# Kernel optimization log

Hardware: AMD Instinct MI355X
Metric: run time of the kernel (lower is better)

## Reference

```python
import jax, jax.numpy as jnp
import numpy as np

B, N_HOP, N_MEM, DIM = 1024, 2, 32, 64


def setup_inputs() -> dict:
    key = jax.random.key(0)
    ks = jax.random.split(key, 8)
    # Xavier-ish scales for linear weights
    def xav(k, shape):
        fan_in = shape[-1]
        return jax.random.normal(k, shape, dtype=jnp.float32) * (1.0 / np.sqrt(fan_in))
    return {
        "hs": jax.random.normal(ks[0], (B, N_HOP, N_MEM, DIM), dtype=jnp.float32),
        "Rs": jax.random.normal(ks[1], (B, N_HOP, N_MEM, DIM, DIM), dtype=jnp.float32) * (1.0 / np.sqrt(DIM)),
        "ts": jax.random.normal(ks[2], (B, N_HOP, N_MEM, DIM), dtype=jnp.float32),
        "vs": jax.random.normal(ks[3], (B, DIM), dtype=jnp.float32),
        "W1_w": xav(ks[4], (DIM, 4 * DIM)),
        "W1_b": jnp.zeros((DIM,), dtype=jnp.float32),
        "W2_w": xav(ks[5], (1, DIM)),
        "W2_b": jnp.zeros((1,), dtype=jnp.float32),
        "Wmem_w": xav(ks[6], (N_HOP, DIM, 3 * DIM)),
        "Wmem_b": jnp.zeros((N_HOP, DIM), dtype=jnp.float32),
        "z_w": xav(ks[7], (DIM, 2 * DIM)),
        "z_b": jnp.zeros((DIM,), dtype=jnp.float32),
    }


def reference(hs, Rs, ts, vs, W1_w, W1_b, W2_w, W2_b, Wmem_w, Wmem_b, z_w, z_b):
    """Faithful RippleNetPlus.forward (eval mode: dropout is identity)."""
    M = vs  # prev_mem
    o = vs  # v passed into EpisodicMemory each hop
    n_hop = hs.shape[1]
    for hop in range(n_hop):
        R = Rs[:, hop]   # [B, M, D, D]
        h = hs[:, hop]   # [B, M, D]
        t = ts[:, hop]   # [B, M, D]
        # batched GEMV replacing the B*n_memory Python-loop matmuls
        Rh = jnp.einsum('bmde,bme->bmd', R, h)  # [B, M, D]
        v = o[:, None, :]       # [B, 1, D]
        pm = M[:, None, :]      # [B, 1, D]
        z = jnp.concatenate(
            [Rh * v, Rh * pm, jnp.abs(Rh - v), jnp.abs(Rh - pm)], axis=-1)  # [B, M, 4D]
        hcode = jnp.tanh(jnp.einsum('bmf,df->bmd', z, W1_w) + W1_b)
        Z = (jnp.einsum('bmd,od->bmo', hcode, W2_w) + W2_b)[..., 0]  # [B, M]
        g = jax.nn.softmax(Z, axis=1)[..., None]                     # [B, M, 1]
        o_new = jnp.sum(t * g, axis=1)                               # [B, D]
        concat = jnp.concatenate([M, o_new, o], axis=1)              # [B, 3D]
        M = jax.nn.relu(concat @ Wmem_w[hop].T + Wmem_b[hop])
        o = o_new
    # AnswerModule
    u = jnp.concatenate([M, vs], axis=1) @ z_w.T + z_b  # [B, D]
    return jnp.sum(vs * u, axis=1)  # [B]
```

## Files before the change

### kernel.cpp

```cpp
#include <hip/hip_runtime.h>
#include <math.h>

#define NHOP 2
#define MEM 32
#define DIM 64

typedef __attribute__((ext_vector_type(8))) short short8v;
typedef __attribute__((ext_vector_type(4))) float f32x4;

__device__ __forceinline__ float fast_tanh(float x) {
    const float e = __expf(2.f * x);
    return 1.f - 2.f / (e + 1.f);
}

__device__ __forceinline__ short bf16b(float x) {
    union { float f; unsigned u; } c; c.f = x;
    const unsigned r = c.u + 0x7fffu + ((c.u >> 16) & 1u);
    return (short)(r >> 16);
}

__global__ __launch_bounds__(256, 3) void ripple_fwd(
    const float* __restrict__ hs,
    const float* __restrict__ Rs,
    const float* __restrict__ ts,
    const float* __restrict__ vs,
    const float* __restrict__ W1_w,
    const float* __restrict__ W1_b,
    const float* __restrict__ W2_w,
    const float* __restrict__ W2_b,
    const float* __restrict__ Wmem_w,
    const float* __restrict__ Wmem_b,
    const float* __restrict__ z_w,
    const float* __restrict__ z_b,
    float* __restrict__ out)
{
    __shared__ uint4 W1B[32 * 64];
    __shared__ float Rh_sm[MEM][68];
    __shared__ float part[4][32][17];
    __shared__ float M_sm[DIM], o_sm[DIM], onew_sm[DIM], vs_sm[DIM];
    __shared__ float Zp[2][MEM];
    __shared__ float cvec[128];

    const int b   = blockIdx.x;
    const int tid = threadIdx.x;
    const int l   = tid & 63;
    const int wv  = tid >> 6;

    #pragma unroll
    for (int t = 0; t < 8; ++t) {
        const int s    = t * 256 + tid;
        const int frag = s >> 6, ll = s & 63;
        const int kt = frag >> 2, nt = frag & 3;
        const int n  = nt * 16 + (ll & 15);
        const int f0 = kt * 32 + (ll >> 4) * 8;
        const float4 wa = *reinterpret_cast<const float4*>(W1_w + n * 256 + f0);
        const float4 wb = *reinterpret_cast<const float4*>(W1_w + n * 256 + f0 + 4);
        short8v v;
        v[0] = bf16b(wa.x); v[1] = bf16b(wa.y); v[2] = bf16b(wa.z); v[3] = bf16b(wa.w);
        v[4] = bf16b(wb.x); v[5] = bf16b(wb.y); v[6] = bf16b(wb.z); v[7] = bf16b(wb.w);
        *reinterpret_cast<short8v*>(&W1B[s]) = v;
    }
    if (tid < DIM) {
        cvec[tid]      = W1_b[tid];
        cvec[64 + tid] = W2_w[tid];
        const float v = vs[b * DIM + tid];
        M_sm[tid] = v; o_sm[tid] = v; vs_sm[tid] = v;
    }

    const int s4   = l & 15;
    const int dq   = l >> 4;
    const int rrow = l & 31;
    const int hi   = l >> 5;

    for (int hop = 0; hop < NHOP; ++hop) {
        const float* __restrict__ Rbase = Rs + (size_t)(b * NHOP + hop) * MEM * DIM * DIM;
        const float* __restrict__ hbase = hs + (size_t)(b * NHOP + hop) * MEM * DIM;
        const float* __restrict__ tbase = ts + (size_t)(b * NHOP + hop) * MEM * DIM;

        #pragma unroll 2
        for (int k = 0; k < 8; ++k) {
            const int m = k * 4 + wv;
            const float* __restrict__ Rm = Rbase + (size_t)m * DIM * DIM;
            const float4 hv = *reinterpret_cast<const float4*>(hbase + m * DIM + 4 * s4);
            #pragma unroll
            for (int half = 0; half < 2; ++half) {
                #pragma unroll
                for (int i = 0; i < 8; ++i) {
                    const float4 r = *reinterpret_cast<const float4*>(
                        Rm + (half * 8 + i) * 256 + 4 * l);
                    const float p = r.x*hv.x + r.y*hv.y + r.z*hv.z + r.w*hv.w;
                    part[wv][4 * i + dq][s4] = p;
                }
                float a = 0.f;
                #pragma unroll
                for (int j = 0; j < 8; ++j)
                    a += part[wv][rrow][hi * 8 + j];
                a += __shfl_xor(a, 32);
                if (l < 32) Rh_sm[m][half * 32 + rrow] = a;
            }
        }
        __syncthreads();

        {
            const int g   = l >> 4;
            const int col = l & 15;
            const int mt  = wv & 1;
            const int nh  = wv >> 1;
            const int m   = mt * 16 + col;
            f32x4 acc0 = {0.f, 0.f, 0.f, 0.f};
            f32x4 acc1 = {0.f, 0.f, 0.f, 0.f};
            #pragma unroll
            for (int kt = 0; kt < 8; ++kt) {
                const int part2 = kt >> 1;
                const int e0 = (kt & 1) * 32 + g * 8;
                const float4 r0 = *reinterpret_cast<const float4*>(&Rh_sm[m][e0]);
                const float4 r1 = *reinterpret_cast<const float4*>(&Rh_sm[m][e0 + 4]);
                const float* vsrc = (part2 & 1) ? M_sm : o_sm;
                const float4 q0 = *reinterpret_cast<const float4*>(vsrc + e0);
                const float4 q1 = *reinterpret_cast<const float4*>(vsrc + e0 + 4);
                float zz[8];
                if (part2 < 2) {
                    zz[0] = r0.x*q0.x; zz[1] = r0.y*q0.y; zz[2] = r0.z*q0.z; zz[3] = r0.w*q0.w;
                    zz[4] = r1.x*q1.x; zz[5] = r1.y*q1.y; zz[6] = r1.z*q1.z; zz[7] = r1.w*q1.w;
                } else {
                    zz[0] = fabsf(r0.x-q0.x); zz[1] = fabsf(r0.y-q0.y);
                    zz[2] = fabsf(r0.z-q0.z); zz[3] = fabsf(r0.w-q0.w);
                    zz[4] = fabsf(r1.x-q1.x); zz[5] = fabsf(r1.y-q1.y);
                    zz[6] = fabsf(r1.z-q1.z); zz[7] = fabsf(r1.w-q1.w);
                }
                short8v a;
                a[0] = bf16b(zz[0]); a[1] = bf16b(zz[1]); a[2] = bf16b(zz[2]); a[3] = bf16b(zz[3]);
                a[4] = bf16b(zz[4]); a[5] = bf16b(zz[5]); a[6] = bf16b(zz[6]); a[7] = bf16b(zz[7]);
                const short8v b0 = *reinterpret_cast<const short8v*>(&W1B[(kt * 4 + nh * 2 + 0) * 64 + l]);
                const short8v b1 = *reinterpret_cast<const short8v*>(&W1B[(kt * 4 + nh * 2 + 1) * 64 + l]);
                acc0 = __builtin_amdgcn_mfma_f32_16x16x32_bf16(a, b0, acc0, 0, 0, 0);
                acc1 = __builtin_amdgcn_mfma_f32_16x16x32_bf16(a, b1, acc1, 0, 0, 0);
            }
            const int n0 = (nh * 2 + 0) * 16 + col;
            const int n1 = (nh * 2 + 1) * 16 + col;
            const float b1a = cvec[n0], b1b = cvec[n1];
            const float w2a = cvec[64 + n0], w2b = cvec[64 + n1];
            float pz[4];
            #pragma unroll
            for (int r = 0; r < 4; ++r)
                pz[r] = fast_tanh(acc0[r] + b1a) * w2a + fast_tanh(acc1[r] + b1b) * w2b;
            #pragma unroll
            for (int s = 1; s < 16; s <<= 1) {
                pz[0] += __shfl_xor(pz[0], s, 64);
                pz[1] += __shfl_xor(pz[1], s, 64);
                pz[2] += __shfl_xor(pz[2], s, 64);
                pz[3] += __shfl_xor(pz[3], s, 64);
            }
            if (col == 0) {
                #pragma unroll
                for (int r = 0; r < 4; ++r)
                    Zp[nh][mt * 16 + 4 * g + r] = pz[r];
            }
        }
        __syncthreads();

        if (tid < DIM) {
            float mx = -1e30f;
            #pragma unroll
            for (int m = 0; m < MEM; ++m) mx = fmaxf(mx, Zp[0][m] + Zp[1][m]);
            float s = 0.f, accn = 0.f;
            #pragma unroll
            for (int m = 0; m < MEM; ++m) {
                const float e = __expf(Zp[0][m] + Zp[1][m] - mx);
                s += e;
                accn = fmaf(tbase[m * DIM + tid], e, accn);
            }
            const float onew = accn / s;
            onew_sm[tid] = onew;

            const float* __restrict__ Wm = Wmem_w + (size_t)(hop * DIM + tid) * 192;
            float acc2 = Wmem_b[hop * DIM + tid];
            #pragma unroll
            for (int k = 0; k < 16; ++k) {
                const float4 w = *reinterpret_cast<const float4*>(Wm + 4 * k);
                acc2 += w.x * M_sm[4*k] + w.y * M_sm[4*k+1] + w.z * M_sm[4*k+2] + w.w * M_sm[4*k+3];
            }
            #pragma unroll
            for (int k = 0; k < 16; ++k) {
                const float4 w = *reinterpret_cast<const float4*>(Wm + 64 + 4 * k);
                acc2 += w.x * onew_sm[4*k] + w.y * onew_sm[4*k+1] + w.z * onew_sm[4*k+2] + w.w * onew_sm[4*k+3];
            }
            #pragma unroll
            for (int k = 0; k < 16; ++k) {
                const float4 w = *reinterpret_cast<const float4*>(Wm + 128 + 4 * k);
                acc2 += w.x * o_sm[4*k] + w.y * o_sm[4*k+1] + w.z * o_sm[4*k+2] + w.w * o_sm[4*k+3];
            }
            M_sm[tid] = fmaxf(acc2, 0.f);
            o_sm[tid] = onew;
        }
        if (hop == 0) __syncthreads();
    }

    if (tid < DIM) {
        const float* __restrict__ zr = z_w + (size_t)tid * 128;
        float u = z_b[tid];
        #pragma unroll
        for (int k = 0; k < 16; ++k) {
            const float4 w = *reinterpret_cast<const float4*>(zr + 4 * k);
            u += w.x * M_sm[4*k] + w.y * M_sm[4*k+1] + w.z * M_sm[4*k+2] + w.w * M_sm[4*k+3];
        }
        #pragma unroll
        for (int k = 0; k < 16; ++k) {
            const float4 w = *reinterpret_cast<const float4*>(zr + 64 + 4 * k);
            u += w.x * vs_sm[4*k] + w.y * vs_sm[4*k+1] + w.z * vs_sm[4*k+2] + w.w * vs_sm[4*k+3];
        }
        float r = vs_sm[tid] * u;
        #pragma unroll
        for (int s = 1; s < 64; s <<= 1) r += __shfl_xor(r, s, 64);
        if (tid == 0) out[b] = r;
    }
}

extern "C" void kernel_launch(void* const* d_in, const int* in_sizes, int n_in,
                              void* d_out, int out_size, void* d_ws, size_t ws_size,
                              hipStream_t stream)
{
    const float* hs     = (const float*)d_in[0];
    const float* Rs     = (const float*)d_in[1];
    const float* ts     = (const float*)d_in[2];
    const float* vs     = (const float*)d_in[3];
    const float* W1_w   = (const float*)d_in[4];
    const float* W1_b   = (const float*)d_in[5];
    const float* W2_w   = (const float*)d_in[6];
    const float* W2_b   = (const float*)d_in[7];
    const float* Wmem_w = (const float*)d_in[8];
    const float* Wmem_b = (const float*)d_in[9];
    const float* z_w    = (const float*)d_in[10];
    const float* z_b    = (const float*)d_in[11];
    float* out = (float*)d_out;

    const int B = out_size;
    ripple_fwd<<<B, 256, 0, stream>>>(hs, Rs, ts, vs, W1_w, W1_b, W2_w, W2_b,
                                      Wmem_w, Wmem_b, z_w, z_b, out);
}
```

Before: 195.3 us.

## Overlap hop-0 memory update with hop-1 Rh GEMV via warp specialization

```diff
diff --git a/kernel.cpp b/kernel.cpp
--- a/kernel.cpp
+++ b/kernel.cpp
@@ -36,7 +36,7 @@
 {
     __shared__ uint4 W1B[32 * 64];
     __shared__ float Rh_sm[MEM][68];
-    __shared__ float part[4][32][17];
+    __shared__ __align__(16) float part[4][32][20];
     __shared__ float M_sm[DIM], o_sm[DIM], onew_sm[DIM], vs_sm[DIM];
     __shared__ float Zp[2][MEM];
     __shared__ float cvec[128];
@@ -72,93 +72,92 @@
     const int rrow = l & 31;
     const int hi   = l >> 5;
 
-    for (int hop = 0; hop < NHOP; ++hop) {
-        const float* __restrict__ Rbase = Rs + (size_t)(b * NHOP + hop) * MEM * DIM * DIM;
-        const float* __restrict__ hbase = hs + (size_t)(b * NHOP + hop) * MEM * DIM;
-        const float* __restrict__ tbase = ts + (size_t)(b * NHOP + hop) * MEM * DIM;
-
-        #pragma unroll 2
-        for (int k = 0; k < 8; ++k) {
-            const int m = k * 4 + wv;
-            const float* __restrict__ Rm = Rbase + (size_t)m * DIM * DIM;
-            const float4 hv = *reinterpret_cast<const float4*>(hbase + m * DIM + 4 * s4);
-            #pragma unroll
-            for (int half = 0; half < 2; ++half) {
-                #pragma unroll
-                for (int i = 0; i < 8; ++i) {
-                    const float4 r = *reinterpret_cast<const float4*>(
-                        Rm + (half * 8 + i) * 256 + 4 * l);
-                    const float p = r.x*hv.x + r.y*hv.y + r.z*hv.z + r.w*hv.w;
-                    part[wv][4 * i + dq][s4] = p;
-                }
-                float a = 0.f;
-                #pragma unroll
-                for (int j = 0; j < 8; ++j)
-                    a += part[wv][rrow][hi * 8 + j];
-                a += __shfl_xor(a, 32);
-                if (l < 32) Rh_sm[m][half * 32 + rrow] = a;
-            }
-        }
-        __syncthreads();
-
-        {
-            const int g   = l >> 4;
-            const int col = l & 15;
-            const int mt  = wv & 1;
-            const int nh  = wv >> 1;
-            const int m   = mt * 16 + col;
-            f32x4 acc0 = {0.f, 0.f, 0.f, 0.f};
-            f32x4 acc1 = {0.f, 0.f, 0.f, 0.f};
-            #pragma unroll
-            for (int kt = 0; kt < 8; ++kt) {
-                const int part2 = kt >> 1;
-                const int e0 = (kt & 1) * 32 + g * 8;
-                const float4 r0 = *reinterpret_cast<const float4*>(&Rh_sm[m][e0]);
-                const float4 r1 = *reinterpret_cast<const float4*>(&Rh_sm[m][e0 + 4]);
-                const float* vsrc = (part2 & 1) ? M_sm : o_sm;
-                const float4 q0 = *reinterpret_cast<const float4*>(vsrc + e0);
-                const float4 q1 = *reinterpret_cast<const float4*>(vsrc + e0 + 4);
-                float zz[8];
-                if (part2 < 2) {
-                    zz[0] = r0.x*q0.x; zz[1] = r0.y*q0.y; zz[2] = r0.z*q0.z; zz[3] = r0.w*q0.w;
-                    zz[4] = r1.x*q1.x; zz[5] = r1.y*q1.y; zz[6] = r1.z*q1.z; zz[7] = r1.w*q1.w;
-                } else {
-                    zz[0] = fabsf(r0.x-q0.x); zz[1] = fabsf(r0.y-q0.y);
-                    zz[2] = fabsf(r0.z-q0.z); zz[3] = fabsf(r0.w-q0.w);
-                    zz[4] = fabsf(r1.x-q1.x); zz[5] = fabsf(r1.y-q1.y);
-                    zz[6] = fabsf(r1.z-q1.z); zz[7] = fabsf(r1.w-q1.w);
-                }
-                short8v a;
-                a[0] = bf16b(zz[0]); a[1] = bf16b(zz[1]); a[2] = bf16b(zz[2]); a[3] = bf16b(zz[3]);
-                a[4] = bf16b(zz[4]); a[5] = bf16b(zz[5]); a[6] = bf16b(zz[6]); a[7] = bf16b(zz[7]);
-                const short8v b0 = *reinterpret_cast<const short8v*>(&W1B[(kt * 4 + nh * 2 + 0) * 64 + l]);
-                const short8v b1 = *reinterpret_cast<const short8v*>(&W1B[(kt * 4 + nh * 2 + 1) * 64 + l]);
-                acc0 = __builtin_amdgcn_mfma_f32_16x16x32_bf16(a, b0, acc0, 0, 0, 0);
-                acc1 = __builtin_amdgcn_mfma_f32_16x16x32_bf16(a, b1, acc1, 0, 0, 0);
-            }
-            const int n0 = (nh * 2 + 0) * 16 + col;
-            const int n1 = (nh * 2 + 1) * 16 + col;
-            const float b1a = cvec[n0], b1b = cvec[n1];
-            const float w2a = cvec[64 + n0], w2b = cvec[64 + n1];
-            float pz[4];
+    const float* __restrict__ Rbase0 = Rs + (size_t)(b * NHOP + 0) * MEM * DIM * DIM;
+    const float* __restrict__ Rbase1 = Rs + (size_t)(b * NHOP + 1) * MEM * DIM * DIM;
+    const float* __restrict__ hbase0 = hs + (size_t)(b * NHOP + 0) * MEM * DIM;
+    const float* __restrict__ hbase1 = hs + (size_t)(b * NHOP + 1) * MEM * DIM;
+    const float* __restrict__ tbase0 = ts + (size_t)(b * NHOP + 0) * MEM * DIM;
+    const float* __restrict__ tbase1 = ts + (size_t)(b * NHOP + 1) * MEM * DIM;
+
+    auto p1 = [&](const float* __restrict__ Rbase, const float* __restrict__ hbase,
+                  const int m) {
+        const float* __restrict__ Rm = Rbase + (size_t)m * DIM * DIM;
+        const float4 hv = *reinterpret_cast<const float4*>(hbase + m * DIM + 4 * s4);
+        #pragma unroll
+        for (int half = 0; half < 2; ++half) {
+            #pragma unroll
+            for (int i = 0; i < 8; ++i) {
+                const f32x4* rp = reinterpret_cast<const f32x4*>(
+                    Rm + (half * 8 + i) * 256 + 4 * l);
+                const f32x4 r = __builtin_nontemporal_load(rp);
+                part[wv][4 * i + dq][s4] = r.x*hv.x + r.y*hv.y + r.z*hv.z + r.w*hv.w;
+            }
+            const float4 pa = *reinterpret_cast<const float4*>(&part[wv][rrow][hi * 8]);
+            const float4 pb = *reinterpret_cast<const float4*>(&part[wv][rrow][hi * 8 + 4]);
+            float a = ((pa.x + pa.y) + (pa.z + pa.w)) + ((pb.x + pb.y) + (pb.z + pb.w));
+            a += __shfl_xor(a, 32);
+            if (l < 32) Rh_sm[m][half * 32 + rrow] = a;
+        }
+    };
+
+    auto p2 = [&]() {
+        const int g   = l >> 4;
+        const int col = l & 15;
+        const int mt  = wv & 1;
+        const int nh  = wv >> 1;
+        const int m   = mt * 16 + col;
+        f32x4 acc0 = {0.f, 0.f, 0.f, 0.f};
+        f32x4 acc1 = {0.f, 0.f, 0.f, 0.f};
+        #pragma unroll
+        for (int kt = 0; kt < 8; ++kt) {
+            const int pt = kt >> 1;
+            const int e0 = (kt & 1) * 32 + g * 8;
+            const float4 r0 = *reinterpret_cast<const float4*>(&Rh_sm[m][e0]);
+            const float4 r1 = *reinterpret_cast<const float4*>(&Rh_sm[m][e0 + 4]);
+            const float* vsrc = (pt & 1) ? M_sm : o_sm;
+            const float4 q0 = *reinterpret_cast<const float4*>(vsrc + e0);
+            const float4 q1 = *reinterpret_cast<const float4*>(vsrc + e0 + 4);
+            float zz[8];
+            if (pt < 2) {
+                zz[0] = r0.x*q0.x; zz[1] = r0.y*q0.y; zz[2] = r0.z*q0.z; zz[3] = r0.w*q0.w;
+                zz[4] = r1.x*q1.x; zz[5] = r1.y*q1.y; zz[6] = r1.z*q1.z; zz[7] = r1.w*q1.w;
+            } else {
+                zz[0] = fabsf(r0.x-q0.x); zz[1] = fabsf(r0.y-q0.y);
+                zz[2] = fabsf(r0.z-q0.z); zz[3] = fabsf(r0.w-q0.w);
+                zz[4] = fabsf(r1.x-q1.x); zz[5] = fabsf(r1.y-q1.y);
+                zz[6] = fabsf(r1.z-q1.z); zz[7] = fabsf(r1.w-q1.w);
+            }
+            short8v a;
+            a[0] = bf16b(zz[0]); a[1] = bf16b(zz[1]); a[2] = bf16b(zz[2]); a[3] = bf16b(zz[3]);
+            a[4] = bf16b(zz[4]); a[5] = bf16b(zz[5]); a[6] = bf16b(zz[6]); a[7] = bf16b(zz[7]);
+            const short8v b0 = *reinterpret_cast<const short8v*>(&W1B[(kt * 4 + nh * 2 + 0) * 64 + l]);
+            const short8v b1 = *reinterpret_cast<const short8v*>(&W1B[(kt * 4 + nh * 2 + 1) * 64 + l]);
+            acc0 = __builtin_amdgcn_mfma_f32_16x16x32_bf16(a, b0, acc0, 0, 0, 0);
+            acc1 = __builtin_amdgcn_mfma_f32_16x16x32_bf16(a, b1, acc1, 0, 0, 0);
+        }
+        const int n0 = (nh * 2 + 0) * 16 + col;
+        const int n1 = (nh * 2 + 1) * 16 + col;
+        const float b1a = cvec[n0], b1b = cvec[n1];
+        const float w2a = cvec[64 + n0], w2b = cvec[64 + n1];
+        float pz[4];
+        #pragma unroll
+        for (int r = 0; r < 4; ++r)
+            pz[r] = fast_tanh(acc0[r] + b1a) * w2a + fast_tanh(acc1[r] + b1b) * w2b;
+        #pragma unroll
+        for (int s = 1; s < 16; s <<= 1) {
+            pz[0] += __shfl_xor(pz[0], s, 64);
+            pz[1] += __shfl_xor(pz[1], s, 64);
+            pz[2] += __shfl_xor(pz[2], s, 64);
+            pz[3] += __shfl_xor(pz[3], s, 64);
+        }
+        if (col == 0) {
             #pragma unroll
             for (int r = 0; r < 4; ++r)
-                pz[r] = fast_tanh(acc0[r] + b1a) * w2a + fast_tanh(acc1[r] + b1b) * w2b;
-            #pragma unroll
-            for (int s = 1; s < 16; s <<= 1) {
-                pz[0] += __shfl_xor(pz[0], s, 64);
-                pz[1] += __shfl_xor(pz[1], s, 64);
-                pz[2] += __shfl_xor(pz[2], s, 64);
-                pz[3] += __shfl_xor(pz[3], s, 64);
-            }
-            if (col == 0) {
-                #pragma unroll
-                for (int r = 0; r < 4; ++r)
-                    Zp[nh][mt * 16 + 4 * g + r] = pz[r];
-            }
-        }
-        __syncthreads();
-
+                Zp[nh][mt * 16 + 4 * g + r] = pz[r];
+        }
+    };
+
+    auto cluster = [&](const int hop, const float* __restrict__ tbase) {
         if (tid < DIM) {
             float mx = -1e30f;
             #pragma unroll
@@ -193,26 +192,51 @@
             M_sm[tid] = fmaxf(acc2, 0.f);
             o_sm[tid] = onew;
         }
-        if (hop == 0) __syncthreads();
-    }
-
-    if (tid < DIM) {
-        const float* __restrict__ zr = z_w + (size_t)tid * 128;
-        float u = z_b[tid];
-        #pragma unroll
-        for (int k = 0; k < 16; ++k) {
-            const float4 w = *reinterpret_cast<const float4*>(zr + 4 * k);
-            u += w.x * M_sm[4*k] + w.y * M_sm[4*k+1] + w.z * M_sm[4*k+2] + w.w * M_sm[4*k+3];
-        }
-        #pragma unroll
-        for (int k = 0; k < 16; ++k) {
-            const float4 w = *reinterpret_cast<const float4*>(zr + 64 + 4 * k);
-            u += w.x * vs_sm[4*k] + w.y * vs_sm[4*k+1] + w.z * vs_sm[4*k+2] + w.w * vs_sm[4*k+3];
-        }
-        float r = vs_sm[tid] * u;
-        #pragma unroll
-        for (int s = 1; s < 64; s <<= 1) r += __shfl_xor(r, s, 64);
-        if (tid == 0) out[b] = r;
+    };
+
+    #pragma unroll 2
+    for (int k = 0; k < 8; ++k)
+        p1(Rbase0, hbase0, k * 4 + wv);
+    __syncthreads();
+
+    p2();
+    __syncthreads();
+
+    if (wv == 0) {
+        cluster(0, tbase0);
+        #pragma unroll 2
+        for (int j = 0; j < 8; ++j)
+            p1(Rbase1, hbase1, 24 + j);
+    } else {
+        #pragma unroll 2
+        for (int j = 0; j < 8; ++j)
+            p1(Rbase1, hbase1, (wv - 1) * 8 + j);
+    }
+    __syncthreads();
+
+    p2();
+    __syncthreads();
+
+    if (wv == 0) {
+        cluster(1, tbase1);
+        if (tid < DIM) {
+            const float* __restrict__ zr = z_w + (size_t)tid * 128;
+            float u = z_b[tid];
+            #pragma unroll
+            for (int k = 0; k < 16; ++k) {
+                const float4 w = *reinterpret_cast<const float4*>(zr + 4 * k);
+                u += w.x * M_sm[4*k] + w.y * M_sm[4*k+1] + w.z * M_sm[4*k+2] + w.w * M_sm[4*k+3];
+            }
+            #pragma unroll
+            for (int k = 0; k < 16; ++k) {
+                const float4 w = *reinterpret_cast<const float4*>(zr + 64 + 4 * k);
+                u += w.x * vs_sm[4*k] + w.y * vs_sm[4*k+1] + w.z * vs_sm[4*k+2] + w.w * vs_sm[4*k+3];
+            }
+            float r = vs_sm[tid] * u;
+            #pragma unroll
+            for (int s = 1; s < 64; s <<= 1) r += __shfl_xor(r, s, 64);
+            if (tid == 0) out[b] = r;
+        }
     }
 }
 
```

After: 176.9 us. 1.1x faster.
